# Optimization experiments

Measured on AMD Instinct MI355X. Metric: run time of the kernel, lower is better.

Reference implementation:

```python
import jax, jax.numpy as jnp
import numpy as np
import math

B, S, D = 2, 2048, 2048
H, KV = 16, 4
HD = D // H          # 128
REP = H // KV        # 4


def setup_inputs() -> dict:
    key = jax.random.key(0)
    ks = jax.random.split(key, 6)
    x = jax.random.normal(ks[0], (B, S, D), dtype=jnp.float32)
    wq = jax.random.normal(ks[1], (D, D), dtype=jnp.float32) * (D ** -0.5)
    wk = jax.random.normal(ks[2], (KV * HD, D), dtype=jnp.float32) * (D ** -0.5)
    wv = jax.random.normal(ks[3], (KV * HD, D), dtype=jnp.float32) * (D ** -0.5)
    wo = jax.random.normal(ks[4], (D, D), dtype=jnp.float32) * (D ** -0.5)
    # RoPE frequencies: theta_i = 10000^(-2i/hd), angle = pos * theta_i
    inv_freq = 1.0 / (10000.0 ** (np.arange(0, HD, 2, dtype=np.float32) / HD))
    angles = np.arange(S, dtype=np.float32)[:, None] * inv_freq[None, :]  # [S, HD/2]
    freqs_cos = jnp.asarray(np.cos(angles), dtype=jnp.float32)
    freqs_sin = jnp.asarray(np.sin(angles), dtype=jnp.float32)
    return {"x": x, "wq": wq, "wk": wk, "wv": wv, "wo": wo,
            "freqs_cos": freqs_cos, "freqs_sin": freqs_sin}


def _rope(t, cos, sin):
    # t: [B, S, h, HD]; cos/sin: [S, HD/2]; complex multiply on (even, odd) pairs
    tr = t.reshape(*t.shape[:-1], HD // 2, 2)
    t0, t1 = tr[..., 0], tr[..., 1]
    c = cos[None, :, None, :]
    s = sin[None, :, None, :]
    o0 = t0 * c - t1 * s
    o1 = t0 * s + t1 * c
    return jnp.stack([o0, o1], axis=-1).reshape(t.shape)


def reference(x, wq, wk, wv, wo, freqs_cos, freqs_sin):
    # projections (torch Linear: y = x @ W.T)
    q = jnp.einsum('bsd,ed->bse', x, wq).reshape(B, S, H, HD)
    k = jnp.einsum('bsd,ed->bse', x, wk).reshape(B, S, KV, HD)
    v = jnp.einsum('bsd,ed->bse', x, wv).reshape(B, S, KV, HD)
    q = _rope(q, freqs_cos, freqs_sin)
    k = _rope(k, freqs_cos, freqs_sin)
    # GQA: repeat each kv head REP times -> [B, S, H, HD]
    k = jnp.repeat(k, REP, axis=2)
    v = jnp.repeat(v, REP, axis=2)
    # [B, H, S, HD]
    q = q.transpose(0, 2, 1, 3)
    k = k.transpose(0, 2, 1, 3)
    v = v.transpose(0, 2, 1, 3)
    scores = jnp.einsum('bhqd,bhkd->bhqk', q, k) * (1.0 / math.sqrt(HD))
    # faithful to torch: tril then masked_fill(scores == 0, -inf)
    scores = jnp.tril(scores)
    scores = jnp.where(scores == 0.0, -jnp.inf, scores)
    attn = jax.nn.softmax(scores, axis=-1)
    out = jnp.einsum('bhqk,bhkd->bhqd', attn, v)
    out = out.transpose(0, 2, 1, 3).reshape(B, S, D)
    return jnp.einsum('bsd,ed->bse', out, wo)
```

## Files before the change

kernel.cpp:

```cpp
#include <hip/hip_runtime.h>
#include <stdint.h>

#define B_ 2
#define S_ 2048
#define D_ 2048
#define NH 16
#define NKV 4
#define HD_ 128

typedef unsigned short u16;
typedef unsigned int u32;
typedef __attribute__((ext_vector_type(8))) __bf16 bf16x8;
typedef __attribute__((ext_vector_type(4))) float f32x4;
typedef __attribute__((ext_vector_type(16))) float f32x16;
typedef __attribute__((ext_vector_type(4))) unsigned int u32x4;
typedef __attribute__((ext_vector_type(8))) unsigned short ushort8v;

__device__ __forceinline__ u16 f2bf(float f) {
  u32 u = __builtin_bit_cast(u32, f);
  u32 r = (u + 0x7FFFu + ((u >> 16) & 1u)) >> 16;
  return (u16)r;
}
__device__ __forceinline__ float bf2f(u16 h) {
  return __builtin_bit_cast(float, ((u32)h) << 16);
}
__device__ __forceinline__ u32 cvtpk(float lo, float hi) {
  u32 r;
  asm("v_cvt_pk_bf16_f32 %0, %1, %2" : "=v"(r) : "v"(lo), "v"(hi));
  return r;
}
__device__ __forceinline__ f32x16 zero16() {
  f32x16 v;
#pragma unroll
  for (int i = 0; i < 16; ++i) v[i] = 0.f;
  return v;
}

__device__ __forceinline__ void gld_lds16(const void* g, void* l) {
  __builtin_amdgcn_global_load_lds(
      (const __attribute__((address_space(1))) void*)g,
      (__attribute__((address_space(3))) void*)l, 16, 0, 0);
}

__global__ __launch_bounds__(256) void k_f2b(const float* __restrict__ src,
                                             u16* __restrict__ dst, int n8) {
  int i = blockIdx.x * 256 + threadIdx.x;
  if (i >= n8) return;
  const float4* s = (const float4*)src + 2 * (size_t)i;
  float4 a = s[0], b = s[1];
  ushort8v o;
  o[0] = f2bf(a.x); o[1] = f2bf(a.y); o[2] = f2bf(a.z); o[3] = f2bf(a.w);
  o[4] = f2bf(b.x); o[5] = f2bf(b.y); o[6] = f2bf(b.z); o[7] = f2bf(b.w);
  *((ushort8v*)dst + i) = o;
}

template <typename OT>
__device__ __forceinline__ void cstore(OT* C, size_t i, float v);
template <> __device__ __forceinline__ void cstore<float>(float* C, size_t i, float v) { C[i] = v; }
template <> __device__ __forceinline__ void cstore<u16>(u16* C, size_t i, float v) { C[i] = f2bf(v); }

template <typename OT>
__device__ __forceinline__ void gemm_core(char* lds, const u16* __restrict__ A,
                                          const u16* __restrict__ W, OT* __restrict__ C,
                                          int N, int K, int bx, int by) {
  char* ldsA = lds;
  char* ldsB = lds + 16384;
  const int tid = threadIdx.x;
  const int lane = tid & 63;
  const int wave = tid >> 6;
  const int m0 = bx * 128, n0 = by * 128;
  const int wm = (wave >> 1) * 64, wn = (wave & 1) * 64;
  f32x4 acc[4][4];
#pragma unroll
  for (int i = 0; i < 4; ++i)
#pragma unroll
    for (int j = 0; j < 4; ++j) acc[i][j] = f32x4{0.f, 0.f, 0.f, 0.f};
  const size_t Kb2 = (size_t)K * 2;
  int rowS[4], colS[4];
#pragma unroll
  for (int j = 0; j < 4; ++j) {
    int plin = j * 4096 + tid * 16;
    int o = plin ^ (((plin >> 7) & 7) << 4);
    rowS[j] = o >> 7;
    colS[j] = o & 127;
  }
  for (int kt = 0; kt < K; kt += 64) {
#pragma unroll
    for (int j = 0; j < 4; ++j) {
      gld_lds16((const char*)A + (size_t)(m0 + rowS[j]) * Kb2 + (size_t)kt * 2 + colS[j],
                ldsA + j * 4096 + wave * 1024);
      gld_lds16((const char*)W + (size_t)(n0 + rowS[j]) * Kb2 + (size_t)kt * 2 + colS[j],
                ldsB + j * 4096 + wave * 1024);
    }
    __syncthreads();
#pragma unroll
    for (int kk = 0; kk < 2; ++kk) {
      const int colb = kk * 64 + ((lane >> 4) << 4);
      bf16x8 af[4], bfv[4];
#pragma unroll
      for (int mi = 0; mi < 4; ++mi) {
        int row = wm + mi * 16 + (lane & 15);
        af[mi] = *(const bf16x8*)(ldsA + (row << 7) + (colb ^ ((row & 7) << 4)));
      }
#pragma unroll
      for (int ni = 0; ni < 4; ++ni) {
        int row = wn + ni * 16 + (lane & 15);
        bfv[ni] = *(const bf16x8*)(ldsB + (row << 7) + (colb ^ ((row & 7) << 4)));
      }
#pragma unroll
      for (int mi = 0; mi < 4; ++mi)
#pragma unroll
        for (int ni = 0; ni < 4; ++ni)
          acc[mi][ni] = __builtin_amdgcn_mfma_f32_16x16x32_bf16(af[mi], bfv[ni], acc[mi][ni], 0, 0, 0);
    }
    __syncthreads();
  }
#pragma unroll
  for (int mi = 0; mi < 4; ++mi)
#pragma unroll
    for (int ni = 0; ni < 4; ++ni) {
      const int n = n0 + wn + ni * 16 + (lane & 15);
#pragma unroll
      for (int r = 0; r < 4; ++r) {
        const int m = m0 + wm + mi * 16 + ((lane >> 4) << 2) + r;
        cstore(C, (size_t)m * N + n, acc[mi][ni][r]);
      }
    }
}

__global__ __launch_bounds__(256) void k_gemm_bf(const u16* __restrict__ A,
    const u16* __restrict__ W, u16* __restrict__ C, int N, int K) {
  __shared__ char lds[32768];
  gemm_core(lds, A, W, C, N, K, blockIdx.x, blockIdx.y);
}

__global__ __launch_bounds__(512, 1) void k_gemm_out(const u16* __restrict__ A,
    const u16* __restrict__ W, float* __restrict__ C, int N, int K) {
  __shared__ char lds[2][49152];
  const int tid = threadIdx.x, lane = tid & 63, wave = tid >> 6;
  const int wm = wave >> 2, wn = wave & 3;
  const int m0 = blockIdx.x * 256, n0 = blockIdx.y * 128;
  const size_t Kb2 = (size_t)K * 2;
  f32x4 acc[8][2];
#pragma unroll
  for (int mi = 0; mi < 8; ++mi)
#pragma unroll
    for (int ni = 0; ni < 2; ++ni) acc[mi][ni] = f32x4{0.f, 0.f, 0.f, 0.f};
  int rA[4], cA[4], rB[2], cB[2];
#pragma unroll
  for (int j = 0; j < 4; ++j) {
    int p = j * 8192 + tid * 16;
    int o = p ^ (((p >> 7) & 7) << 4);
    rA[j] = o >> 7; cA[j] = o & 127;
  }
#pragma unroll
  for (int j = 0; j < 2; ++j) {
    int p = j * 8192 + tid * 16;
    int o = p ^ (((p >> 7) & 7) << 4);
    rB[j] = o >> 7; cB[j] = o & 127;
  }
  auto stage = [&](int t) {
    char* dst = &lds[t & 1][0];
    const char* As = (const char*)A + (size_t)t * 128;
    const char* Ws = (const char*)W + (size_t)t * 128;
#pragma unroll
    for (int j = 0; j < 4; ++j)
      gld_lds16(As + (size_t)(m0 + rA[j]) * Kb2 + cA[j], dst + j * 8192 + tid * 16);
#pragma unroll
    for (int j = 0; j < 2; ++j)
      gld_lds16(Ws + (size_t)(n0 + rB[j]) * Kb2 + cB[j], dst + 32768 + j * 8192 + tid * 16);
  };
  stage(0);
  __syncthreads();
  const int nt = K >> 6;
  for (int t = 0; t < nt; ++t) {
    if (t + 1 < nt) stage(t + 1);
    const char* buf = &lds[t & 1][0];
#pragma unroll
    for (int kk = 0; kk < 2; ++kk) {
      const int cb = kk * 64 + ((lane >> 4) << 4);
      bf16x8 af[8], bfr[2];
#pragma unroll
      for (int mi = 0; mi < 8; ++mi) {
        int r = wm * 128 + mi * 16 + (lane & 15);
        af[mi] = *(const bf16x8*)(buf + (r << 7) + (cb ^ ((r & 7) << 4)));
      }
#pragma unroll
      for (int ni = 0; ni < 2; ++ni) {
        int r = wn * 32 + ni * 16 + (lane & 15);
        bfr[ni] = *(const bf16x8*)(buf + 32768 + (r << 7) + (cb ^ ((r & 7) << 4)));
      }
      __builtin_amdgcn_s_setprio(1);
#pragma unroll
      for (int mi = 0; mi < 8; ++mi)
#pragma unroll
        for (int ni = 0; ni < 2; ++ni)
          acc[mi][ni] = __builtin_amdgcn_mfma_f32_16x16x32_bf16(af[mi], bfr[ni], acc[mi][ni], 0, 0, 0);
      __builtin_amdgcn_s_setprio(0);
    }
    __syncthreads();
  }
#pragma unroll
  for (int mi = 0; mi < 8; ++mi)
#pragma unroll
    for (int ni = 0; ni < 2; ++ni) {
      const int n = n0 + wn * 32 + ni * 16 + (lane & 15);
#pragma unroll
      for (int r = 0; r < 4; ++r) {
        const int m = m0 + wm * 128 + mi * 16 + ((lane >> 4) << 2) + r;
        C[(size_t)m * N + n] = acc[mi][ni][r];
      }
    }
}

__global__ __launch_bounds__(256) void k_rope(const u16* __restrict__ src,
    u16* __restrict__ dst, const float* __restrict__ fc, const float* __restrict__ fs,
    int nh, int lognh, int dorope, int total, int rs, int coloff, float smul) {
  int idx = blockIdx.x * 256 + threadIdx.x;
  if (idx >= total) return;
  const int q4 = idx & 15;
  const int rest = idx >> 4;
  const int hidx = rest & (nh - 1);
  const int t = rest >> lognh;
  const int b = t >> 11, s = t & 2047;
  ushort8v ev = *(const ushort8v*)(src + (size_t)t * rs + coloff + hidx * HD_ + q4 * 8);
  float e[8];
#pragma unroll
  for (int j = 0; j < 8; ++j) e[j] = bf2f(ev[j]);
  float o[8];
  if (dorope) {
    float4 c4 = *(const float4*)(fc + s * 64 + q4 * 4);
    float4 s4 = *(const float4*)(fs + s * 64 + q4 * 4);
    float cc[4] = {c4.x, c4.y, c4.z, c4.w};
    float ss[4] = {s4.x, s4.y, s4.z, s4.w};
#pragma unroll
    for (int j = 0; j < 4; ++j) {
      o[2 * j]     = (e[2 * j] * cc[j] - e[2 * j + 1] * ss[j]) * smul;
      o[2 * j + 1] = (e[2 * j] * ss[j] + e[2 * j + 1] * cc[j]) * smul;
    }
  } else {
#pragma unroll
    for (int j = 0; j < 8; ++j) o[j] = e[j] * smul;
  }
  ushort8v w;
#pragma unroll
  for (int j = 0; j < 8; ++j) w[j] = f2bf(o[j]);
  *(ushort8v*)(dst + (((size_t)(b * nh + hidx)) * S_ + s) * HD_ + q4 * 8) = w;
}

__global__ __launch_bounds__(256, 2) void k_attn(const u16* __restrict__ qkv,
    const u16* __restrict__ Kt, const float* __restrict__ fc,
    const float* __restrict__ fs, u16* __restrict__ O) {
  __shared__ char kls[2][16384];
  __shared__ char vls[2][16384];
  const int h = blockIdx.x, b = blockIdx.y;
  const int z = blockIdx.z;
  const int qtb = (z < 8) ? (15 - z) : (z - 8);
  const int tid = threadIdx.x, lane = tid & 63, wave = tid >> 6;
  const int ql = lane & 31, g = lane >> 5;
  const int kvh = h >> 2;
  const u16* Kb = Kt + ((size_t)(b * NKV + kvh)) * S_ * HD_;
  const int q0 = qtb * 128, qw0 = q0 + wave * 32;
  const int qme = qw0 + ql;
  int kRowS[4], kColS[4];
#pragma unroll
  for (int j = 0; j < 4; ++j) {
    int plin = j * 4096 + tid * 16;
    int o = plin ^ (((plin >> 8) & 7) << 4);
    kRowS[j] = o >> 8;
    kColS[j] = o & 255;
  }
  const int kp = tid & 31, hb = (tid >> 5) * 16;
  const u16* Vsrc = qkv + 2560 + kvh * HD_;
  auto loadV = [&](int tn, u32* vr0, u32* vr1) {
    const u16* vp = Vsrc + (size_t)(b * S_ + tn * 64 + 2 * kp) * 3072 + hb;
    const u32* r0 = (const u32*)vp;
    const u32* r1 = (const u32*)(vp + 3072);
#pragma unroll
    for (int wd = 0; wd < 8; ++wd) { vr0[wd] = r0[wd]; vr1[wd] = r1[wd]; }
  };
  auto writeV = [&](char* vn, const u32* vr0, const u32* vr1) {
#pragma unroll
    for (int wd = 0; wd < 8; ++wd) {
      u32 v0 = vr0[wd], v1 = vr1[wd];
      u32 lo = (v0 & 0xFFFFu) | (v1 << 16);
      u32 hi = (v0 >> 16) | (v1 & 0xFFFF0000u);
      int hd0 = hb + 2 * wd, hd1 = hd0 + 1;
      *(u32*)(vn + hd0 * 128 + ((4 * kp) ^ ((hd0 & 7) << 4))) = lo;
      *(u32*)(vn + hd1 * 128 + ((4 * kp) ^ ((hd1 & 7) << 4))) = hi;
    }
  };

#pragma unroll
  for (int j = 0; j < 4; ++j)
    gld_lds16((const char*)Kb + (size_t)kRowS[j] * 256 + kColS[j],
              &kls[0][0] + j * 4096 + wave * 1024);
  u32 pv0[8], pv1[8];
  loadV(0, pv0, pv1);

  const float QS = 0.08838834764831845f * 1.4426950408889634f;
  const u16* Qrow = qkv + (size_t)(b * S_ + qme) * 3072 + h * HD_;
  bf16x8 qf[8];
#pragma unroll
  for (int kk = 0; kk < 8; ++kk) {
    ushort8v ev = __builtin_bit_cast(ushort8v, *(const bf16x8*)(Qrow + kk * 16 + g * 8));
    int pb = (kk * 16 + g * 8) >> 1;
    float4 c4 = *(const float4*)(fc + (size_t)qme * 64 + pb);
    float4 s4 = *(const float4*)(fs + (size_t)qme * 64 + pb);
    float cc[4] = {c4.x * QS, c4.y * QS, c4.z * QS, c4.w * QS};
    float ss[4] = {s4.x * QS, s4.y * QS, s4.z * QS, s4.w * QS};
    ushort8v w;
#pragma unroll
    for (int j = 0; j < 4; ++j) {
      float e0 = bf2f(ev[2 * j]), e1 = bf2f(ev[2 * j + 1]);
      w[2 * j]     = f2bf(e0 * cc[j] - e1 * ss[j]);
      w[2 * j + 1] = f2bf(e0 * ss[j] + e1 * cc[j]);
    }
    qf[kk] = __builtin_bit_cast(bf16x8, w);
  }
  writeV(&vls[0][0], pv0, pv1);
  __syncthreads();

  f32x16 oacc[4];
#pragma unroll
  for (int th = 0; th < 4; ++th) oacc[th] = zero16();
  float mrun = -1e30f, lrun = 0.0f;
  const int nt = 2 * qtb + 2;

  int cur = 0;
  for (int t = 0; t < nt; ++t) {
    const int kv0 = t * 64;
    const bool haveNext = (t + 1 < nt);
    u32 vr0[8], vr1[8];
    if (haveNext) {
      const int kvn = kv0 + 64;
#pragma unroll
      for (int j = 0; j < 4; ++j)
        gld_lds16((const char*)Kb + (size_t)(kvn + kRowS[j]) * 256 + kColS[j],
                  &kls[cur ^ 1][0] + j * 4096 + wave * 1024);
      loadV(t + 1, vr0, vr1);
    }
    if (kv0 <= qw0 + 31) {
      const char* kcur = &kls[cur][0];
      const char* vcur = &vls[cur][0];
      f32x16 c0 = zero16(), c1 = zero16();
      __builtin_amdgcn_s_setprio(1);
#pragma unroll
      for (int kk = 0; kk < 8; ++kk) {
        const int sw = (kk * 32 + 16 * g) ^ ((ql & 7) << 4);
        bf16x8 kf0 = *(const bf16x8*)(kcur + (ql << 8) + sw);
        bf16x8 kf1 = *(const bf16x8*)(kcur + ((32 + ql) << 8) + sw);
        c0 = __builtin_amdgcn_mfma_f32_32x32x16_bf16(kf0, qf[kk], c0, 0, 0, 0);
        c1 = __builtin_amdgcn_mfma_f32_32x32x16_bf16(kf1, qf[kk], c1, 0, 0, 0);
      }
      __builtin_amdgcn_s_setprio(0);
      const bool diag = (kv0 + 63 > qw0);
      float mt = -1e30f;
      if (diag) {
#pragma unroll
        for (int r = 0; r < 16; ++r) {
          float s0 = c0[r], s1 = c1[r];
          int kb = kv0 + (r & 3) + ((r >> 2) << 3) + 4 * g;
          if (kb > qme) s0 = -1e30f;
          if (kb + 32 > qme) s1 = -1e30f;
          c0[r] = s0; c1[r] = s1;
          mt = fmaxf(mt, fmaxf(s0, s1));
        }
      } else {
#pragma unroll
        for (int r = 0; r < 16; ++r)
          mt = fmaxf(mt, fmaxf(c0[r], c1[r]));
      }
      mt = fmaxf(mt, __shfl_xor(mt, 32));
      if (!__all(mt <= mrun + 8.0f)) {
        float mnew = fmaxf(mrun, mt);
        float alpha = exp2f(mrun - mnew);
        lrun *= alpha;
        mrun = mnew;
#pragma unroll
        for (int r = 0; r < 16; ++r) {
          float av = __shfl(alpha, 36 * g + (r & 3) + ((r >> 2) << 3));
          oacc[0][r] *= av; oacc[1][r] *= av;
          oacc[2][r] *= av; oacc[3][r] *= av;
        }
      }
      float lt = 0.0f;
#pragma unroll
      for (int r = 0; r < 16; ++r) {
        float p0 = exp2f(c0[r] - mrun);
        float p1 = exp2f(c1[r] - mrun);
        c0[r] = p0; c1[r] = p1;
        lt += p0 + p1;
      }
      lt += __shfl_xor(lt, 32);
      lrun += lt;
      u32 paw[4][4];
#pragma unroll
      for (int a = 0; a < 2; ++a) {
        {
          u32 X = cvtpk(c0[8 * a + 0], c0[8 * a + 1]);
          u32 Y = cvtpk(c0[8 * a + 2], c0[8 * a + 3]);
          u32 Z = cvtpk(c0[8 * a + 4], c0[8 * a + 5]);
          u32 W = cvtpk(c0[8 * a + 6], c0[8 * a + 7]);
          u32 S1 = g ? X : Z, S2 = g ? Y : W;
          u32 R1 = (u32)__shfl_xor((int)S1, 32), R2 = (u32)__shfl_xor((int)S2, 32);
          paw[a][0] = g ? R1 : X; paw[a][1] = g ? R2 : Y;
          paw[a][2] = g ? Z : R1; paw[a][3] = g ? W : R2;
        }
        {
          u32 X = cvtpk(c1[8 * a + 0], c1[8 * a + 1]);
          u32 Y = cvtpk(c1[8 * a + 2], c1[8 * a + 3]);
          u32 Z = cvtpk(c1[8 * a + 4], c1[8 * a + 5]);
          u32 W = cvtpk(c1[8 * a + 6], c1[8 * a + 7]);
          u32 S1 = g ? X : Z, S2 = g ? Y : W;
          u32 R1 = (u32)__shfl_xor((int)S1, 32), R2 = (u32)__shfl_xor((int)S2, 32);
          paw[2 + a][0] = g ? R1 : X; paw[2 + a][1] = g ? R2 : Y;
          paw[2 + a][2] = g ? Z : R1; paw[2 + a][3] = g ? W : R2;
        }
      }
      __builtin_amdgcn_s_setprio(1);
#pragma unroll
      for (int ks = 0; ks < 4; ++ks) {
        bf16x8 pf = __builtin_bit_cast(bf16x8,
            u32x4{paw[ks][0], paw[ks][1], paw[ks][2], paw[ks][3]});
        const int cb = (32 * ks + 16 * g) ^ ((ql & 7) << 4);
#pragma unroll
        for (int th = 0; th < 4; ++th) {
          bf16x8 vf = *(const bf16x8*)(vcur + ((th * 32 + ql) << 7) + cb);
          oacc[th] = __builtin_amdgcn_mfma_f32_32x32x16_bf16(pf, vf, oacc[th], 0, 0, 0);
        }
      }
      __builtin_amdgcn_s_setprio(0);
    }
    if (haveNext) writeV(&vls[cur ^ 1][0], vr0, vr1);
    __syncthreads();
    cur ^= 1;
  }
#pragma unroll
  for (int r = 0; r < 16; ++r) {
    float lr = __shfl(lrun, 36 * g + (r & 3) + ((r >> 2) << 3));
    float li = 1.0f / lr;
    int q = qw0 + (r & 3) + ((r >> 2) << 3) + 4 * g;
    size_t rowo = (size_t)(b * S_ + q) * D_ + h * HD_ + ql;
#pragma unroll
    for (int th = 0; th < 4; ++th)
      O[rowo + 32 * th] = f2bf(oacc[th][r] * li);
  }
}

extern "C" void kernel_launch(void* const* d_in, const int* in_sizes, int n_in,
                              void* d_out, int out_size, void* d_ws, size_t ws_size,
                              hipStream_t stream) {
  const float* x  = (const float*)d_in[0];
  const float* wq = (const float*)d_in[1];
  const float* wk = (const float*)d_in[2];
  const float* wv = (const float*)d_in[3];
  const float* wv_ = wv;
  const float* wo = (const float*)d_in[4];
  const float* fc = (const float*)d_in[5];
  const float* fs = (const float*)d_in[6];
  (void)wv_;
  float* out = (float*)d_out;
  char* ws = (char*)d_ws;
  const size_t MB = 1ull << 20;
  u16* xb    = (u16*)(ws);
  u16* wqkv  = (u16*)(ws + 16 * MB);
  u16* wob   = (u16*)(ws + 28 * MB);
  u16* qkvbf = (u16*)(ws + 36 * MB);
  u16* attb  = (u16*)(ws);
  u16* Kb    = (u16*)(ws + 16 * MB);

  auto cv = [&](const float* s, u16* d, int n) {
    int n8 = n / 8;
    k_f2b<<<dim3((n8 + 255) / 256), dim3(256), 0, stream>>>(s, d, n8);
  };
  cv(x,  xb,   B_ * S_ * D_);
  cv(wq, wqkv,             D_ * D_);
  cv(wk, wqkv + 2048*2048, 512 * D_);
  cv(wv, wqkv + 2560*2048, 512 * D_);
  cv(wo, wob,  D_ * D_);

  k_gemm_bf<<<dim3(32, 24), dim3(256), 0, stream>>>(xb, wqkv, qkvbf, 3072, D_);

  k_rope<<<dim3(1024), dim3(256), 0, stream>>>(qkvbf, Kb, fc, fs, 4, 2, 1,
                                               B_ * S_ * 4 * 16, 3072, 2048, 1.0f);

  k_attn<<<dim3(NH, B_, 16), dim3(256), 0, stream>>>(qkvbf, Kb, fc, fs, attb);

  k_gemm_out<<<dim3(16, 16), dim3(512), 0, stream>>>(attb, wob, out, D_, D_);
}
```

Measured before the change: 238.9 us.

## Fuse fp32-to-bf16 conversions into one launch and pre-pack V contiguously

The five separate fp32-to-bf16 conversion launches become a single kernel that picks its source tensor by index range, which removes launch overhead and tail gaps. A second k_rope pass, with rotation disabled, copies V out of the strided qkv buffer into a contiguous [B,KV,S,HD] layout. The attention kernel then reads V rows with a 256-byte stride instead of 6144 bytes, so the loads are better coalesced. The cost is one extra kernel launch plus an extra read and write of V. The gemm template is also inlined, which is cleanup only.

Measured after the change: 220.9 us. 7.5% less time.

```diff
diff --git a/kernel.cpp b/kernel.cpp
--- a/kernel.cpp
+++ b/kernel.cpp
@@ -42,33 +42,39 @@
       (__attribute__((address_space(3))) void*)l, 16, 0, 0);
 }
 
-__global__ __launch_bounds__(256) void k_f2b(const float* __restrict__ src,
-                                             u16* __restrict__ dst, int n8) {
-  int i = blockIdx.x * 256 + threadIdx.x;
-  if (i >= n8) return;
-  const float4* s = (const float4*)src + 2 * (size_t)i;
-  float4 a = s[0], b = s[1];
+__device__ __forceinline__ void cv8(const float* s, u16* d, int i) {
+  const float4* sp = (const float4*)s + 2 * (size_t)i;
+  float4 a = sp[0], b = sp[1];
   ushort8v o;
   o[0] = f2bf(a.x); o[1] = f2bf(a.y); o[2] = f2bf(a.z); o[3] = f2bf(a.w);
   o[4] = f2bf(b.x); o[5] = f2bf(b.y); o[6] = f2bf(b.z); o[7] = f2bf(b.w);
-  *((ushort8v*)dst + i) = o;
-}
-
-template <typename OT>
-__device__ __forceinline__ void cstore(OT* C, size_t i, float v);
-template <> __device__ __forceinline__ void cstore<float>(float* C, size_t i, float v) { C[i] = v; }
-template <> __device__ __forceinline__ void cstore<u16>(u16* C, size_t i, float v) { C[i] = f2bf(v); }
-
-template <typename OT>
-__device__ __forceinline__ void gemm_core(char* lds, const u16* __restrict__ A,
-                                          const u16* __restrict__ W, OT* __restrict__ C,
-                                          int N, int K, int bx, int by) {
+  *((ushort8v*)d + i) = o;
+}
+__global__ __launch_bounds__(256) void k_f2b_all(const float* __restrict__ x,
+    const float* __restrict__ wq, const float* __restrict__ wk,
+    const float* __restrict__ wv, const float* __restrict__ wo,
+    u16* __restrict__ xb, u16* __restrict__ wqkv, u16* __restrict__ wob) {
+  int i = blockIdx.x * 256 + threadIdx.x;
+  if (i < 1048576) { cv8(x, xb, i); return; }
+  i -= 1048576;
+  if (i < 524288) { cv8(wq, wqkv, i); return; }
+  i -= 524288;
+  if (i < 131072) { cv8(wk, wqkv + 2048 * 2048, i); return; }
+  i -= 131072;
+  if (i < 131072) { cv8(wv, wqkv + 2560 * 2048, i); return; }
+  i -= 131072;
+  if (i < 524288) cv8(wo, wob, i);
+}
+
+__global__ __launch_bounds__(256) void k_gemm_bf(const u16* __restrict__ A,
+    const u16* __restrict__ W, u16* __restrict__ C, int N, int K) {
+  __shared__ char lds[32768];
   char* ldsA = lds;
   char* ldsB = lds + 16384;
   const int tid = threadIdx.x;
   const int lane = tid & 63;
   const int wave = tid >> 6;
-  const int m0 = bx * 128, n0 = by * 128;
+  const int m0 = blockIdx.x * 128, n0 = blockIdx.y * 128;
   const int wm = (wave >> 1) * 64, wn = (wave & 1) * 64;
   f32x4 acc[4][4];
 #pragma unroll
@@ -123,15 +129,9 @@
 #pragma unroll
       for (int r = 0; r < 4; ++r) {
         const int m = m0 + wm + mi * 16 + ((lane >> 4) << 2) + r;
-        cstore(C, (size_t)m * N + n, acc[mi][ni][r]);
-      }
-    }
-}
-
-__global__ __launch_bounds__(256) void k_gemm_bf(const u16* __restrict__ A,
-    const u16* __restrict__ W, u16* __restrict__ C, int N, int K) {
-  __shared__ char lds[32768];
-  gemm_core(lds, A, W, C, N, K, blockIdx.x, blockIdx.y);
+        C[(size_t)m * N + n] = f2bf(acc[mi][ni][r]);
+      }
+    }
 }
 
 __global__ __launch_bounds__(512, 1) void k_gemm_out(const u16* __restrict__ A,
@@ -249,8 +249,9 @@
 }
 
 __global__ __launch_bounds__(256, 2) void k_attn(const u16* __restrict__ qkv,
-    const u16* __restrict__ Kt, const float* __restrict__ fc,
-    const float* __restrict__ fs, u16* __restrict__ O) {
+    const u16* __restrict__ Kt, const u16* __restrict__ Vt,
+    const float* __restrict__ fc, const float* __restrict__ fs,
+    u16* __restrict__ O) {
   __shared__ char kls[2][16384];
   __shared__ char vls[2][16384];
   const int h = blockIdx.x, b = blockIdx.y;
@@ -260,6 +261,7 @@
   const int ql = lane & 31, g = lane >> 5;
   const int kvh = h >> 2;
   const u16* Kb = Kt + ((size_t)(b * NKV + kvh)) * S_ * HD_;
+  const u16* Vb = Vt + ((size_t)(b * NKV + kvh)) * S_ * HD_;
   const int q0 = qtb * 128, qw0 = q0 + wave * 32;
   const int qme = qw0 + ql;
   int kRowS[4], kColS[4];
@@ -271,11 +273,10 @@
     kColS[j] = o & 255;
   }
   const int kp = tid & 31, hb = (tid >> 5) * 16;
-  const u16* Vsrc = qkv + 2560 + kvh * HD_;
   auto loadV = [&](int tn, u32* vr0, u32* vr1) {
-    const u16* vp = Vsrc + (size_t)(b * S_ + tn * 64 + 2 * kp) * 3072 + hb;
+    const u16* vp = Vb + (size_t)(tn * 64 + 2 * kp) * HD_ + hb;
     const u32* r0 = (const u32*)vp;
-    const u32* r1 = (const u32*)(vp + 3072);
+    const u32* r1 = (const u32*)(vp + HD_);
 #pragma unroll
     for (int wd = 0; wd < 8; ++wd) { vr0[wd] = r0[wd]; vr1[wd] = r1[wd]; }
   };
@@ -455,11 +456,9 @@
   const float* wq = (const float*)d_in[1];
   const float* wk = (const float*)d_in[2];
   const float* wv = (const float*)d_in[3];
-  const float* wv_ = wv;
   const float* wo = (const float*)d_in[4];
   const float* fc = (const float*)d_in[5];
   const float* fs = (const float*)d_in[6];
-  (void)wv_;
   float* out = (float*)d_out;
   char* ws = (char*)d_ws;
   const size_t MB = 1ull << 20;
@@ -469,23 +468,18 @@
   u16* qkvbf = (u16*)(ws + 36 * MB);
   u16* attb  = (u16*)(ws);
   u16* Kb    = (u16*)(ws + 16 * MB);
-
-  auto cv = [&](const float* s, u16* d, int n) {
-    int n8 = n / 8;
-    k_f2b<<<dim3((n8 + 255) / 256), dim3(256), 0, stream>>>(s, d, n8);
-  };
-  cv(x,  xb,   B_ * S_ * D_);
-  cv(wq, wqkv,             D_ * D_);
-  cv(wk, wqkv + 2048*2048, 512 * D_);
-  cv(wv, wqkv + 2560*2048, 512 * D_);
-  cv(wo, wob,  D_ * D_);
+  u16* Vb    = (u16*)(ws + 20 * MB);
+
+  k_f2b_all<<<dim3(9216), dim3(256), 0, stream>>>(x, wq, wk, wv, wo, xb, wqkv, wob);
 
   k_gemm_bf<<<dim3(32, 24), dim3(256), 0, stream>>>(xb, wqkv, qkvbf, 3072, D_);
 
   k_rope<<<dim3(1024), dim3(256), 0, stream>>>(qkvbf, Kb, fc, fs, 4, 2, 1,
                                                B_ * S_ * 4 * 16, 3072, 2048, 1.0f);
-
-  k_attn<<<dim3(NH, B_, 16), dim3(256), 0, stream>>>(qkvbf, Kb, fc, fs, attb);
+  k_rope<<<dim3(1024), dim3(256), 0, stream>>>(qkvbf, Vb, fc, fs, 4, 2, 0,
+                                               B_ * S_ * 4 * 16, 3072, 2560, 1.0f);
+
+  k_attn<<<dim3(NH, B_, 16), dim3(256), 0, stream>>>(qkvbf, Kb, Vb, fc, fs, attb);
 
   k_gemm_out<<<dim3(16, 16), dim3(512), 0, stream>>>(attb, wob, out, D_, D_);
 }
```
